# Performance work log

Measured on AMD Instinct MI355X. Metric: run time of the kernel, lower is better.

The kernel has to match this reference:

```python
import jax, jax.numpy as jnp
import numpy as np

N_NODES = 65536
N_EDGES = 1048576
DIM = 64
K_HOPS = 3
ALPHA = 0.1


def setup_inputs() -> dict:
    key = jax.random.key(0)
    k1, k2, k3, k4 = jax.random.split(key, 4)
    features = jax.random.normal(k1, (N_NODES, DIM), dtype=jnp.float32)
    src = jax.random.randint(k2, (N_EDGES,), 0, N_NODES, dtype=jnp.int32)
    dst = jax.random.randint(k3, (N_EDGES,), 0, N_NODES, dtype=jnp.int32)
    # attn_fc: Linear(2*out_dim -> 1); store weight as a flat [2*DIM] vector + bias
    attn_w = (jax.random.normal(k4, (2 * DIM,), dtype=jnp.float32) * 0.1)
    attn_b = jnp.zeros((1,), dtype=jnp.float32)
    # temp: APPNP-style coefficients, length k+1
    temp = np.asarray(ALPHA * (1 - ALPHA) ** np.arange(K_HOPS + 1), dtype=np.float32)
    temp[-1] = (1 - ALPHA) ** K_HOPS
    temp = jnp.asarray(temp)
    return {"features": features, "src": src, "dst": dst,
            "attn_w": attn_w, "attn_b": attn_b, "temp": temp}


def reference(features, src, dst, attn_w, attn_b, temp):
    N, D = features.shape
    # split attn weight so we never materialize the [E, 2D] concat
    a_src, a_dst = attn_w[:D], attn_w[D:]
    out = features * temp[0]
    feats = features
    n_hops = temp.shape[0] - 1  # static
    for k in range(n_hops):
        z_src = feats[src]                                  # [E, D] gather
        # e = leaky_relu(attn_fc(concat(z_src, z_dst)))  -> scalar per edge
        e = jax.nn.leaky_relu(z_src @ a_src + feats[dst] @ a_dst + attn_b)  # [E]
        # edge softmax over incoming edges of each dst node
        m = jax.ops.segment_max(e, dst, num_segments=N)     # [N]
        ex = jnp.exp(e - m[dst])                            # [E]
        denom = jax.ops.segment_sum(ex, dst, num_segments=N)  # [N]
        w = ex / denom[dst]                                 # [E]
        # weighted scatter-sum of source features to destinations
        feats = jax.ops.segment_sum(z_src * w[:, None], dst, num_segments=N)  # [N, D]
        out = out + temp[k + 1] * feats
    # NOTE: original module returns features_two (the temp-weighted sum);
    # activation/residual branches modify a dead local and are omitted.
    return out
```

## Files before the change

### kernel.cpp

```cpp
#include <hip/hip_runtime.h>
#include <hip/hip_bf16.h>

#define N_NODES 65536
#define N_EDGES 1048576
#define DIM 64
#define NXCD 8
#define SLOT_CAP 64
#define BIN_BLOCKS 512
#define NBUCKET 512
#define BUCKET_NODES 128
#define CAP_XB 384

typedef float f32x4 __attribute__((ext_vector_type(4)));
typedef unsigned short u16x4 __attribute__((ext_vector_type(4)));
typedef unsigned short u16x8 __attribute__((ext_vector_type(8)));

__device__ __forceinline__ float lrelu(float x) { return x >= 0.f ? x : 0.01f * x; }
__device__ __forceinline__ float bf2f(unsigned short h) {
    return __uint_as_float(((unsigned)h) << 16);
}
__device__ __forceinline__ unsigned short f2bf(float f) {
    return __bfloat16_as_ushort(__float2bfloat16(f));
}

__global__ __launch_bounds__(256) void zero_bins(unsigned* __restrict__ p) {
    p[blockIdx.x * 256 + threadIdx.x] = 0u;
}

__global__ __launch_bounds__(256) void prep_bin512(
    const float* __restrict__ feats, const float* __restrict__ attn_w,
    const int* __restrict__ src, const int* __restrict__ dst,
    float* __restrict__ s0, float* __restrict__ t0,
    unsigned short* __restrict__ fbfF,
    unsigned* __restrict__ bin_cnt,
    unsigned* __restrict__ bucket) {
    __shared__ unsigned lcnt[NBUCKET];
    __shared__ unsigned lbase[NBUCKET];
    int tid = threadIdx.x;
    int lane = tid & 63;
    int g = lane >> 4, l16 = lane & 15;
    int wave_id = blockIdx.x * 4 + (tid >> 6);
    int grp16 = wave_id * 4 + g;

    f32x4 aw_s4 = ((const f32x4*)attn_w)[l16];
    f32x4 aw_t4 = ((const f32x4*)attn_w)[16 + l16];
    #pragma unroll
    for (int it = 0; it < 8; ++it) {
        int node = grp16 + it * 8192;
        f32x4 f4 = ((const f32x4*)feats)[node * 16 + l16];
        u16x4 ub = {f2bf(f4[0]), f2bf(f4[1]), f2bf(f4[2]), f2bf(f4[3])};
        ((u16x4*)fbfF)[node * 16 + l16] = ub;
        float sp = f4[0]*aw_s4[0] + f4[1]*aw_s4[1] + f4[2]*aw_s4[2] + f4[3]*aw_s4[3];
        float tq = f4[0]*aw_t4[0] + f4[1]*aw_t4[1] + f4[2]*aw_t4[2] + f4[3]*aw_t4[3];
        #pragma unroll
        for (int off = 1; off < 16; off <<= 1) {
            sp += __shfl_xor(sp, off);
            tq += __shfl_xor(tq, off);
        }
        if (l16 == 0) { s0[node] = sp; t0[node] = tq; }
    }

    for (int i = tid; i < NBUCKET; i += 256) lcnt[i] = 0;
    __syncthreads();
    unsigned pk[8];
    unsigned short rk[8];
    int ebase = blockIdx.x * 2048;
    #pragma unroll
    for (int it = 0; it < 8; ++it) {
        int e = ebase + it * 256 + tid;
        unsigned d = (unsigned)dst[e], v = (unsigned)src[e];
        pk[it] = (d << 16) | v;
        rk[it] = (unsigned short)atomicAdd(&lcnt[d >> 7], 1u);
    }
    __syncthreads();
    int xcd = blockIdx.x & (NXCD - 1);
    unsigned* bc = bin_cnt + xcd * NBUCKET;
    for (int i = tid; i < NBUCKET; i += 256)
        lbase[i] = atomicAdd(&bc[i], lcnt[i]);
    __syncthreads();
    unsigned* bb = bucket + (size_t)xcd * NBUCKET * CAP_XB;
    #pragma unroll
    for (int it = 0; it < 8; ++it) {
        unsigned bkt = pk[it] >> 23;
        unsigned pos = lbase[bkt] + rk[it];
        if (pos < CAP_XB) bb[bkt * CAP_XB + pos] = pk[it];
    }
}

__global__ __launch_bounds__(256) void scatter_b(
    const unsigned* __restrict__ bucket, const unsigned* __restrict__ bin_cnt,
    unsigned* __restrict__ deg, unsigned short* __restrict__ csr_slot) {
    __shared__ unsigned short slots[BUCKET_NODES * SLOT_CAP];
    __shared__ unsigned cur[BUCKET_NODES];
    int tid = threadIdx.x;
    int b = blockIdx.x;
    unsigned lo = (unsigned)b * BUCKET_NODES;
    if (tid < BUCKET_NODES) cur[tid] = 0;
    __syncthreads();
    #pragma unroll
    for (int x = 0; x < NXCD; ++x) {
        unsigned cnt = min(bin_cnt[x * NBUCKET + b], (unsigned)CAP_XB);
        const unsigned* bb = bucket + ((size_t)x * NBUCKET + b) * CAP_XB;
        for (unsigned i = tid; i < cnt; i += 256) {
            unsigned p = bb[i];
            unsigned rel = (p >> 16) - lo;
            unsigned pos = atomicAdd(&cur[rel], 1u);
            if (pos < SLOT_CAP) slots[(rel << 6) + pos] = (unsigned short)(p & 0xFFFFu);
        }
    }
    __syncthreads();
    u16x4* dv = (u16x4*)(csr_slot + (size_t)lo * SLOT_CAP);
    const u16x4* sv = (const u16x4*)slots;
    for (int j = tid; j < BUCKET_NODES * SLOT_CAP / 4; j += 256)
        dv[j] = sv[j];
    if (tid < BUCKET_NODES) deg[lo + tid] = cur[tid];
}

__global__ __launch_bounds__(256) void node_agg(
    const unsigned short* __restrict__ feats_bf,
    const unsigned short* __restrict__ fbfF,
    const unsigned short* __restrict__ fbfA1,
    const float* __restrict__ s_in, const float* __restrict__ t_in,
    const unsigned* __restrict__ deg_arr, const unsigned short* __restrict__ csr_slot,
    const float* __restrict__ attn_w, const float* __restrict__ attn_b,
    const float* __restrict__ temp, int last,
    unsigned short* __restrict__ feats_out_bf,
    float* __restrict__ s_next, float* __restrict__ t_next,
    float* __restrict__ out) {
    int tid = threadIdx.x;
    int lane = tid & 63;
    int wv = blockIdx.x * 4 + (tid >> 6);
    int g = lane >> 3, l8 = lane & 7;
    int node = wv * 8 + g;

    float tp = t_in[node];
    float b = attn_b[0];
    int deg = min((int)deg_arr[node], SLOT_CAP);

    u16x8 sl = ((const u16x8*)csr_slot)[node * 8 + l8];
    unsigned pk[8];
    #pragma unroll
    for (int je = 0; je < 8; ++je) {
        int idx = l8 * 8 + je;
        bool v = idx < deg;
        int sj = v ? (int)sl[je] : 0;
        float ev = v ? __expf(lrelu(s_in[sj] + tp + b)) : 0.f;
        pk[je] = (((unsigned)f2bf(ev)) << 16) | (unsigned)sj;
    }

    f32x4 accL = {0.f, 0.f, 0.f, 0.f};
    f32x4 accH = {0.f, 0.f, 0.f, 0.f};
    float dn = 0.f;
    const u16x8* feats8 = (const u16x8*)feats_bf;
    int gbase = lane & 56;
    for (int bl = 0; bl * 8 < deg; ++bl) {
        #pragma unroll
        for (int je = 0; je < 8; ++je) {
            unsigned p = __shfl(pk[je], gbase + bl);
            float w = __uint_as_float(p & 0xFFFF0000u);
            u16x8 q = feats8[(p & 0xFFFFu) * 8 + l8];
            accL[0] += w * bf2f(q[0]);
            accL[1] += w * bf2f(q[1]);
            accL[2] += w * bf2f(q[2]);
            accL[3] += w * bf2f(q[3]);
            accH[0] += w * bf2f(q[4]);
            accH[1] += w * bf2f(q[5]);
            accH[2] += w * bf2f(q[6]);
            accH[3] += w * bf2f(q[7]);
            dn += w;
        }
    }
    float inv = (deg > 0) ? 1.f / dn : 0.f;
    f32x4 aL = accL * inv, aH = accH * inv;

    if (!last) {
        u16x8 ub = {f2bf(aL[0]), f2bf(aL[1]), f2bf(aL[2]), f2bf(aL[3]),
                    f2bf(aH[0]), f2bf(aH[1]), f2bf(aH[2]), f2bf(aH[3])};
        ((u16x8*)feats_out_bf)[node * 8 + l8] = ub;
        f32x4 awsL = ((const f32x4*)attn_w)[l8 * 2];
        f32x4 awsH = ((const f32x4*)attn_w)[l8 * 2 + 1];
        f32x4 awtL = ((const f32x4*)attn_w)[16 + l8 * 2];
        f32x4 awtH = ((const f32x4*)attn_w)[16 + l8 * 2 + 1];
        float sp = aL[0]*awsL[0] + aL[1]*awsL[1] + aL[2]*awsL[2] + aL[3]*awsL[3]
                 + aH[0]*awsH[0] + aH[1]*awsH[1] + aH[2]*awsH[2] + aH[3]*awsH[3];
        float tq = aL[0]*awtL[0] + aL[1]*awtL[1] + aL[2]*awtL[2] + aL[3]*awtL[3]
                 + aH[0]*awtH[0] + aH[1]*awtH[1] + aH[2]*awtH[2] + aH[3]*awtH[3];
        #pragma unroll
        for (int off = 1; off < 8; off <<= 1) {
            sp += __shfl_xor(sp, off);
            tq += __shfl_xor(tq, off);
        }
        if (l8 == 0) { s_next[node] = sp; t_next[node] = tq; }
    } else {
        u16x8 fF = ((const u16x8*)fbfF)[node * 8 + l8];
        u16x8 fA1 = ((const u16x8*)fbfA1)[node * 8 + l8];
        u16x8 fA2 = ((const u16x8*)feats_bf)[node * 8 + l8];
        float t0 = temp[0], t1 = temp[1], t2 = temp[2], t3 = temp[3];
        f32x4 oL, oH;
        #pragma unroll
        for (int i = 0; i < 4; ++i) {
            oL[i] = t0 * bf2f(fF[i]) + t1 * bf2f(fA1[i]) + t2 * bf2f(fA2[i]) + t3 * aL[i];
            oH[i] = t0 * bf2f(fF[i + 4]) + t1 * bf2f(fA1[i + 4]) + t2 * bf2f(fA2[i + 4]) + t3 * aH[i];
        }
        ((f32x4*)out)[node * 16 + l8 * 2] = oL;
        ((f32x4*)out)[node * 16 + l8 * 2 + 1] = oH;
    }
}

extern "C" void kernel_launch(void* const* d_in, const int* in_sizes, int n_in,
                              void* d_out, int out_size, void* d_ws, size_t ws_size,
                              hipStream_t stream) {
    const float* features = (const float*)d_in[0];
    const int* src = (const int*)d_in[1];
    const int* dst = (const int*)d_in[2];
    const float* attn_w = (const float*)d_in[3];
    const float* attn_b = (const float*)d_in[4];
    const float* temp = (const float*)d_in[5];
    float* out = (float*)d_out;

    float* s0 = (float*)d_ws;
    float* s1 = s0 + N_NODES;
    float* t0 = s1 + N_NODES;
    float* t1 = t0 + N_NODES;
    unsigned* deg = (unsigned*)(t1 + N_NODES);
    unsigned* bin_cnt = deg + N_NODES;
    unsigned short* csr_slot = (unsigned short*)(bin_cnt + NXCD * NBUCKET);
    unsigned short* fbfF = csr_slot + (size_t)N_NODES * SLOT_CAP;
    unsigned short* fbfA1 = fbfF + (size_t)N_NODES * DIM;
    unsigned* bucket = (unsigned*)(fbfA1 + (size_t)N_NODES * DIM);
    unsigned short* fbfA2 = (unsigned short*)bucket;

    const int AGG_BLOCKS = N_NODES / 32;

    zero_bins<<<16, 256, 0, stream>>>(bin_cnt);
    prep_bin512<<<BIN_BLOCKS, 256, 0, stream>>>(features, attn_w, src, dst,
                                                s0, t0, fbfF, bin_cnt, bucket);
    scatter_b<<<NBUCKET, 256, 0, stream>>>(bucket, bin_cnt, deg, csr_slot);

    node_agg<<<AGG_BLOCKS, 256, 0, stream>>>(fbfF, fbfF, fbfA1, s0, t0, deg, csr_slot,
                                             attn_w, attn_b, temp, 0,
                                             fbfA1, s1, t1, out);
    node_agg<<<AGG_BLOCKS, 256, 0, stream>>>(fbfA1, fbfF, fbfA1, s1, t1, deg, csr_slot,
                                             attn_w, attn_b, temp, 0,
                                             fbfA2, s0, t0, out);
    node_agg<<<AGG_BLOCKS, 256, 0, stream>>>(fbfA2, fbfF, fbfA1, s0, t0, deg, csr_slot,
                                             attn_w, attn_b, temp, 1,
                                             (unsigned short*)0, s1, t1, out);
}
```

Measured before the change: 103.8 us.

## Coarsen edge binning to 64 buckets with local sort for coalesced writes

The binning pass now groups edges into 64 coarse buckets of 1024 nodes instead of 512 buckets of 128. Each block sorts its 2048 edges in shared memory with a prefix-scan so the bucket writes come out contiguous instead of scattered. The scatter kernel now reads the coarse bucket and skips edges outside its 128-node range, so each coarse bucket is read 8 times. The intent is to cut the scattered global writes and global atomics in exchange for that extra read traffic and the extra shared-memory sort.

```diff
diff --git a/kernel.cpp b/kernel.cpp
--- a/kernel.cpp
+++ b/kernel.cpp
@@ -7,9 +7,9 @@
 #define NXCD 8
 #define SLOT_CAP 64
 #define BIN_BLOCKS 512
-#define NBUCKET 512
+#define NBUCKET 64
 #define BUCKET_NODES 128
-#define CAP_XB 384
+#define CAP_XB 2432
 
 typedef float f32x4 __attribute__((ext_vector_type(4)));
 typedef unsigned short u16x4 __attribute__((ext_vector_type(4)));
@@ -27,15 +27,15 @@
     p[blockIdx.x * 256 + threadIdx.x] = 0u;
 }
 
-__global__ __launch_bounds__(256) void prep_bin512(
+__global__ __launch_bounds__(256) void prep_bin64(
     const float* __restrict__ feats, const float* __restrict__ attn_w,
     const int* __restrict__ src, const int* __restrict__ dst,
     float* __restrict__ s0, float* __restrict__ t0,
     unsigned short* __restrict__ fbfF,
     unsigned* __restrict__ bin_cnt,
     unsigned* __restrict__ bucket) {
-    __shared__ unsigned lcnt[NBUCKET];
-    __shared__ unsigned lbase[NBUCKET];
+    __shared__ unsigned lcnt[NBUCKET], lbase[NBUCKET], lstart[NBUCKET];
+    __shared__ unsigned sorted[2048];
     int tid = threadIdx.x;
     int lane = tid & 63;
     int g = lane >> 4, l16 = lane & 15;
@@ -60,7 +60,7 @@
         if (l16 == 0) { s0[node] = sp; t0[node] = tq; }
     }
 
-    for (int i = tid; i < NBUCKET; i += 256) lcnt[i] = 0;
+    if (tid < NBUCKET) lcnt[tid] = 0;
     __syncthreads();
     unsigned pk[8];
     unsigned short rk[8];
@@ -70,20 +70,32 @@
         int e = ebase + it * 256 + tid;
         unsigned d = (unsigned)dst[e], v = (unsigned)src[e];
         pk[it] = (d << 16) | v;
-        rk[it] = (unsigned short)atomicAdd(&lcnt[d >> 7], 1u);
+        rk[it] = (unsigned short)atomicAdd(&lcnt[d >> 10], 1u);
     }
     __syncthreads();
     int xcd = blockIdx.x & (NXCD - 1);
-    unsigned* bc = bin_cnt + xcd * NBUCKET;
-    for (int i = tid; i < NBUCKET; i += 256)
-        lbase[i] = atomicAdd(&bc[i], lcnt[i]);
+    if (tid < 64) {
+        unsigned c = lcnt[tid];
+        unsigned x = c;
+        #pragma unroll
+        for (int off = 1; off < 64; off <<= 1) {
+            unsigned y = __shfl_up(x, off);
+            if (tid >= off) x += y;
+        }
+        lstart[tid] = x - c;
+        lbase[tid] = atomicAdd(&bin_cnt[xcd * NBUCKET + tid], c);
+    }
+    __syncthreads();
+    #pragma unroll
+    for (int it = 0; it < 8; ++it)
+        sorted[lstart[pk[it] >> 26] + rk[it]] = pk[it];
     __syncthreads();
     unsigned* bb = bucket + (size_t)xcd * NBUCKET * CAP_XB;
-    #pragma unroll
-    for (int it = 0; it < 8; ++it) {
-        unsigned bkt = pk[it] >> 23;
-        unsigned pos = lbase[bkt] + rk[it];
-        if (pos < CAP_XB) bb[bkt * CAP_XB + pos] = pk[it];
+    for (int j = tid; j < 2048; j += 256) {
+        unsigned p = sorted[j];
+        unsigned bkt = p >> 26;
+        unsigned pos = lbase[bkt] + ((unsigned)j - lstart[bkt]);
+        if (pos < CAP_XB) bb[bkt * CAP_XB + pos] = p;
     }
 }
 
@@ -94,18 +106,21 @@
     __shared__ unsigned cur[BUCKET_NODES];
     int tid = threadIdx.x;
     int b = blockIdx.x;
+    int pb = b >> 3;
     unsigned lo = (unsigned)b * BUCKET_NODES;
     if (tid < BUCKET_NODES) cur[tid] = 0;
     __syncthreads();
     #pragma unroll
     for (int x = 0; x < NXCD; ++x) {
-        unsigned cnt = min(bin_cnt[x * NBUCKET + b], (unsigned)CAP_XB);
-        const unsigned* bb = bucket + ((size_t)x * NBUCKET + b) * CAP_XB;
+        unsigned cnt = min(bin_cnt[x * NBUCKET + pb], (unsigned)CAP_XB);
+        const unsigned* bb = bucket + ((size_t)x * NBUCKET + pb) * CAP_XB;
         for (unsigned i = tid; i < cnt; i += 256) {
             unsigned p = bb[i];
             unsigned rel = (p >> 16) - lo;
-            unsigned pos = atomicAdd(&cur[rel], 1u);
-            if (pos < SLOT_CAP) slots[(rel << 6) + pos] = (unsigned short)(p & 0xFFFFu);
+            if (rel < (unsigned)BUCKET_NODES) {
+                unsigned pos = atomicAdd(&cur[rel], 1u);
+                if (pos < SLOT_CAP) slots[(rel << 6) + pos] = (unsigned short)(p & 0xFFFFu);
+            }
         }
     }
     __syncthreads();
@@ -224,7 +239,7 @@
     float* t1 = t0 + N_NODES;
     unsigned* deg = (unsigned*)(t1 + N_NODES);
     unsigned* bin_cnt = deg + N_NODES;
-    unsigned short* csr_slot = (unsigned short*)(bin_cnt + NXCD * NBUCKET);
+    unsigned short* csr_slot = (unsigned short*)(bin_cnt + 512);
     unsigned short* fbfF = csr_slot + (size_t)N_NODES * SLOT_CAP;
     unsigned short* fbfA1 = fbfF + (size_t)N_NODES * DIM;
     unsigned* bucket = (unsigned*)(fbfA1 + (size_t)N_NODES * DIM);
@@ -232,10 +247,10 @@
 
     const int AGG_BLOCKS = N_NODES / 32;
 
-    zero_bins<<<16, 256, 0, stream>>>(bin_cnt);
-    prep_bin512<<<BIN_BLOCKS, 256, 0, stream>>>(features, attn_w, src, dst,
-                                                s0, t0, fbfF, bin_cnt, bucket);
-    scatter_b<<<NBUCKET, 256, 0, stream>>>(bucket, bin_cnt, deg, csr_slot);
+    zero_bins<<<2, 256, 0, stream>>>(bin_cnt);
+    prep_bin64<<<BIN_BLOCKS, 256, 0, stream>>>(features, attn_w, src, dst,
+                                               s0, t0, fbfF, bin_cnt, bucket);
+    scatter_b<<<512, 256, 0, stream>>>(bucket, bin_cnt, deg, csr_slot);
 
     node_agg<<<AGG_BLOCKS, 256, 0, stream>>>(fbfF, fbfF, fbfA1, s0, t0, deg, csr_slot,
                                              attn_w, attn_b, temp, 0,
```

Measured after the change: 120.8 us. +16.3%, slower.
